# Kernel optimization log

Hardware: AMD Instinct MI355X
Metric: run time of the kernel (lower is better)

Reference implementation:

```python
import jax, jax.numpy as jnp
import numpy as np

T, B, C = 4, 2, 128
LT, LH, LW = 8, 32, 32
NUM_HEADS = 8
HEAD_DIM = C // NUM_HEADS
THETA = 0.7
V_TH = 1.0
TAU = 2.0  # spikingjelly LIFNode default tau
N_WIN = (2, 2, 2)
TOPK = 4
EPS = 1e-5
ATAN_ALPHA = 2.0  # spikingjelly surrogate.ATan default


@jax.custom_vjp
def spike(x):
    return (x >= 0.0).astype(x.dtype)

def _spike_fwd(x):
    return spike(x), x

def _spike_bwd(x, g):
    s = (jnp.pi / 2.0) * ATAN_ALPHA * x
    return (g * (ATAN_ALPHA / 2.0) / (1.0 + s * s),)

spike.defvjp(_spike_fwd, _spike_bwd)


def lif(x_seq):
    """Multi-step LIF: v'=v+(x-v)/tau, spike at v>=V_TH, hard reset to 0 (detached)."""
    def step(v, x):
        v = v + (x - v) / TAU
        s = spike(v - V_TH)
        v = v * (1.0 - jax.lax.stop_gradient(s))  # detach_reset, v_reset=0
        return v, s
    _, s_seq = jax.lax.scan(step, jnp.zeros_like(x_seq[0]), x_seq)
    return s_seq


def bn(x, gamma, beta):
    # BatchNorm3d(track_running_stats=False) on [T*B, C, D, H, W]: batch stats per channel
    mean = x.mean(axis=(0, 1, 3, 4, 5), keepdims=True)
    var = x.var(axis=(0, 1, 3, 4, 5), keepdims=True)
    shp = (1, 1, -1, 1, 1, 1)
    return (x - mean) * jax.lax.rsqrt(var + EPS) * gamma.reshape(shp) + beta.reshape(shp)


def conv3d(x, w, pad):
    t, b = x.shape[:2]
    y = jax.lax.conv_general_dilated(
        x.reshape((t * b,) + x.shape[2:]), w,
        window_strides=(1, 1, 1), padding=[(pad, pad)] * 3,
        dimension_numbers=('NCDHW', 'OIDHW', 'NCDHW'))
    return y.reshape((t, b) + y.shape[1:])


def cdc_t(x, w):
    out = conv3d(x, w, 1)
    # central-difference temporal term: 1x1x1 conv with summed first/last temporal slices
    kd = w[:, :, 0].sum((-1, -2)) + w[:, :, 2].sum((-1, -2))  # [O, I]
    return out - THETA * jnp.einsum('oi,tbidhw->tbodhw', kd, x)


def to_wins(t):
    wt, wh, ww = N_WIN
    Tn, Bn, Cn, Lt, Lh, Lw = t.shape
    lt, lh, lw = Lt // wt, Lh // wh, Lw // ww
    t = t.reshape(Tn, Bn, Cn, wt, lt, wh, lh, ww, lw)
    t = t.transpose(0, 1, 3, 5, 7, 4, 6, 8, 2)
    return t.reshape(Tn, Bn, wt * wh * ww, lt * lh * lw, Cn)


def setup_inputs() -> dict:
    key = jax.random.key(0)
    ks = jax.random.split(key, 4)
    x = jax.random.normal(ks[0], (T, B, C, LT, LH, LW), jnp.float32)
    qw = jax.random.normal(ks[1], (C, C, 3, 3, 3), jnp.float32) / np.sqrt(C * 27)
    kw = jax.random.normal(ks[2], (C, C), jnp.float32) / np.sqrt(C)
    pw = jax.random.normal(ks[3], (C, C), jnp.float32) / np.sqrt(C)
    ones = jnp.ones((C,), jnp.float32)
    zeros = jnp.zeros((C,), jnp.float32)
    return {"x": x, "qw": qw, "q_gamma": ones, "q_beta": zeros,
            "kw": kw, "k_gamma": ones, "k_beta": zeros,
            "v_gamma": ones, "v_beta": zeros,
            "pw": pw, "p_gamma": ones, "p_beta": zeros}


def reference(x, qw, q_gamma, q_beta, kw, k_gamma, k_beta,
              v_gamma, v_beta, pw, p_gamma, p_beta):
    Tn, Bn, Cn, Lt, Lh, Lw = x.shape
    wt, wh, ww = N_WIN
    num_wins = wt * wh * ww
    lt, lh, lw = Lt // wt, Lh // wh, Lw // ww

    q_real = bn(cdc_t(x, qw), q_gamma, q_beta)
    k_real = bn(jnp.einsum('oi,tbidhw->tbodhw', kw, x), k_gamma, k_beta)

    # region-level routing from pre-spike activations
    q_region = to_wins(q_real).mean(axis=(0, 3))  # [B, W, C]
    k_region = to_wins(k_real).mean(axis=(0, 3))
    a_r = jnp.einsum('bwc,bvc->bwv', q_region, k_region) * (HEAD_DIM ** -0.5)
    k_eff = min(TOPK, num_wins)
    _, idx = jax.lax.top_k(a_r, k_eff)  # [B, W, k]

    q = lif(q_real)
    k = lif(k_real)
    v = lif(bn(x, v_gamma, v_beta))
    q_w = to_wins(q)  # [T,B,W,S,C]
    k_w = to_wins(k)
    v_w = to_wins(v)

    # gather routed windows per (batch, target window), mean-aggregate over top-k
    gather = jax.vmap(lambda src_b, idx_b: src_b[:, idx_b], in_axes=(1, 0), out_axes=1)
    k_agg = gather(k_w, idx).mean(axis=3)  # [T,B,W,S,C]
    v_agg = gather(v_w, idx).mean(axis=3)

    S = q_w.shape[3]
    q_h = q_w.reshape(Tn, Bn, num_wins, S, NUM_HEADS, HEAD_DIM)
    k_h = k_agg.reshape(Tn, Bn, num_wins, S, NUM_HEADS, HEAD_DIM)
    v_h = v_agg.reshape(Tn, Bn, num_wins, S, NUM_HEADS, HEAD_DIM)

    attn = (q_h * k_h).sum(axis=5, keepdims=True)  # [T,B,W,S,H,1]
    attn = lif(attn)
    out = (attn * v_h).reshape(Tn, Bn, num_wins, S, Cn)

    out = out.reshape(Tn, Bn, wt, wh, ww, lt, lh, lw, Cn)
    out = out.transpose(0, 1, 8, 2, 5, 3, 6, 4, 7).reshape(Tn, Bn, Cn, Lt, Lh, Lw)

    out = lif(out)
    out = bn(jnp.einsum('oi,tbidhw->tbodhw', pw, out), p_gamma, p_beta)
    return out
```

## Files before the change

### kernel.cpp

```cpp
#include <hip/hip_runtime.h>

#define TT 4
#define BB 2
#define CC 128
#define DD 8
#define HHH 32
#define WWW 32
#define PP (DD*HHH*WWW)
#define TSTRIDE (BB*CC*PP)
#define NWIN 8
#define SSS 1024
#define NHEAD 8
#define HDIM 16
#define THETA 0.7f
#define VTH 1.0f
#define NPERC (TT*BB*PP)
#define EPSf 1e-5f

typedef unsigned short ushortT;
typedef _Float16 half_t;
typedef _Float16 f16x8 __attribute__((ext_vector_type(8)));
typedef float    f32x16 __attribute__((ext_vector_type(16)));

__global__ __launch_bounds__(256) void prep_wmodT(const float* __restrict__ qw,
                                                  float* __restrict__ wmodT) {
    int oi = blockIdx.x*256 + threadIdx.x;
    if (oi >= CC*CC) return;
    int o  = oi >> 7;
    int ic = oi & 127;
    const float* wp = qw + (size_t)oi*27;
    float kd = 0.f;
    #pragma unroll
    for (int t=0; t<9; t++) kd += wp[t] + wp[18+t];
    #pragma unroll
    for (int t=0; t<27; t++) {
        float v = wp[t] - ((t==13) ? THETA*kd : 0.f);
        wmodT[((size_t)o*27 + t)*CC + ic] = v;
    }
}

__global__ __launch_bounds__(256) void prep_wfrag(const float* __restrict__ wmodT,
                                                  half_t* __restrict__ wfrag) {
    int id = blockIdx.x*256 + threadIdx.x;
    if (id >= 8*27*4*64) return;
    int lane = id & 63;
    int r = id >> 6;
    int m = r & 3; r >>= 2;
    int t = r % 27;
    int kb = r / 27;
    int o   = m*32 + (lane & 31);
    int ic0 = kb*16 + (lane>>5)*8;
    size_t base = ((size_t)(id>>6))*2*64*8 + (size_t)lane*8;
    #pragma unroll
    for (int j=0;j<8;j++){
        float v = wmodT[((size_t)o*27 + t)*CC + ic0 + j];
        half_t h = (half_t)v;
        half_t l = (half_t)(v - (float)h);
        wfrag[base + 0*64*8 + j] = h;
        wfrag[base + 1*64*8 + j] = l;
    }
}

__global__ __launch_bounds__(256) void prep_w1frag(const float* __restrict__ W,
                                                   half_t* __restrict__ frag) {
    int id = blockIdx.x*256 + threadIdx.x;
    if (id >= 2048) return;
    int lane = id & 63;
    int r = id >> 6;
    int m = r & 3;
    int kb = r >> 2;
    int o   = m*32 + (lane & 31);
    int ic0 = kb*16 + (lane>>5)*8;
    size_t base = ((size_t)(kb*4+m))*2*64*8 + (size_t)lane*8;
    #pragma unroll
    for (int j=0;j<8;j++){
        float v = W[(size_t)o*CC + ic0 + j];
        half_t h = (half_t)v;
        half_t l = (half_t)(v - (float)h);
        frag[base + 0*64*8 + j] = h;
        frag[base + 1*64*8 + j] = l;
    }
}

__global__ __launch_bounds__(256) void build_xsplit(const float* __restrict__ x,
                                                    half_t* __restrict__ xsp) {
    int id = blockIdx.x*256 + threadIdx.x;
    if (id >= 8*16*8*34*34) return;
    int wt = id % 34; int r = id/34;
    int hp = r % 34;  r /= 34;
    int dz = r % 8;   r /= 8;
    int icg = r & 15; int tb = r >> 4;
    bool inb = (hp>=1) & (hp<=32) & (wt>=1) & (wt<=32);
    half_t h8[8], l8[8];
    #pragma unroll
    for (int j=0;j<8;j++){
        float v = 0.f;
        if (inb)
            v = x[((size_t)(tb*CC + icg*8+j))*PP + (size_t)dz*1024 + (hp-1)*32 + (wt-1)];
        half_t h = (half_t)v;
        half_t l = (half_t)(v - (float)h);
        h8[j]=h; l8[j]=l;
    }
    #pragma unroll
    for (int sp=0; sp<2; sp++){
        size_t gu = (((((size_t)tb*2 + sp)*16 + icg)*8 + dz)*34 + hp)*34 + wt;
        half_t* dst = xsp + gu*8;
        const half_t* src = (sp==0)?h8:l8;
        #pragma unroll
        for (int j=0;j<8;j++) dst[j] = src[j];
    }
}

__global__ __launch_bounds__(256,2) void conv_mfma2(const half_t* __restrict__ xsp,
                                                    const half_t* __restrict__ wfrag,
                                                    float* __restrict__ y0,
                                                    float* __restrict__ y1) {
    __shared__ half_t slab[3264*8];
    int tid  = threadIdx.x;
    int wid  = tid >> 6;
    int lane = tid & 63;
    int ln   = lane & 31;
    int half_ = lane >> 5;
    int hg = blockIdx.x;
    int dp = blockIdx.y;
    int z  = blockIdx.z;
    int tb = z >> 1, kh = z & 1;
    int H0 = hg*4, d0 = dp*2;
    float* y = kh ? y1 : y0;

    f32x16 acc[2][4];
    #pragma unroll
    for (int dt=0;dt<2;dt++)
        #pragma unroll
        for (int m=0;m<4;m++)
            #pragma unroll
            for (int i=0;i<16;i++) acc[dt][m][i] = 0.f;

    f16x8 ca[4][2];
    #pragma unroll
    for (int m=0;m<4;m++)
        #pragma unroll
        for (int sp=0;sp<2;sp++)
            ca[m][sp] = *(const f16x8*)&wfrag[((((size_t)(kh*4*27)*4 + m)*2+sp)*64 + lane)*8];

    #pragma unroll 1
    for (int kk=0; kk<4; kk++) {
        int kb = kh*4 + kk;
        __syncthreads();
        for (int u = tid; u < 3264; u += 256) {
            int sp  = u / 1632;
            int r   = u - sp*1632;
            int icg = r / 816;
            int p   = r - icg*816;
            int dz  = p / 204;
            int r3  = p - dz*204;
            int hp  = r3 / 34;
            int wt  = r3 - hp*34;
            int dd  = d0 - 1 + dz;
            ulonglong2 v; v.x = 0; v.y = 0;
            if ((unsigned)dd < 8u) {
                size_t gu = (((((size_t)tb*2 + sp)*16 + (kb*2+icg))*8 + dd)*34 + (H0+hp))*34 + wt;
                v = *(const ulonglong2*)&xsp[gu*8];
            }
            *(ulonglong2*)&slab[(size_t)u*8] = v;
        }
        __syncthreads();
        #pragma unroll 1
        for (int t=0; t<27; t++) {
            int dz=t/9; int rr=t-dz*9; int dh=rr/3; int dw=rr-dh*3;
            f16x8 cb[2][2];
            #pragma unroll
            for (int dt=0;dt<2;dt++){
                int bpos = (dt+dz)*204 + (wid+dh)*34 + ln + dw;
                #pragma unroll
                for (int sp=0;sp<2;sp++)
                    cb[dt][sp] = *(const f16x8*)&slab[(size_t)((sp*2+half_)*816 + bpos)*8];
            }
            f16x8 na[4][2];
            int nt  = (t<26)? t+1 : 0;
            int nkb = (t<26)? kb  : ((kk<3)? kb+1 : kb);
            #pragma unroll
            for (int m=0;m<4;m++)
                #pragma unroll
                for (int sp=0;sp<2;sp++)
                    na[m][sp] = *(const f16x8*)&wfrag[((((size_t)(nkb*27+nt)*4+m)*2+sp)*64 + lane)*8];
            #pragma unroll
            for (int dt=0;dt<2;dt++)
                #pragma unroll
                for (int m=0;m<4;m++) acc[dt][m] = __builtin_amdgcn_mfma_f32_32x32x16_f16(ca[m][0], cb[dt][0], acc[dt][m],0,0,0);
            #pragma unroll
            for (int dt=0;dt<2;dt++)
                #pragma unroll
                for (int m=0;m<4;m++) acc[dt][m] = __builtin_amdgcn_mfma_f32_32x32x16_f16(ca[m][0], cb[dt][1], acc[dt][m],0,0,0);
            #pragma unroll
            for (int dt=0;dt<2;dt++)
                #pragma unroll
                for (int m=0;m<4;m++) acc[dt][m] = __builtin_amdgcn_mfma_f32_32x32x16_f16(ca[m][1], cb[dt][0], acc[dt][m],0,0,0);
            #pragma unroll
            for (int dt=0;dt<2;dt++)
                #pragma unroll
                for (int m=0;m<4;m++) acc[dt][m] = __builtin_amdgcn_mfma_f32_32x32x16_f16(ca[m][1], cb[dt][1], acc[dt][m],0,0,0);
            #pragma unroll
            for (int m=0;m<4;m++)
                #pragma unroll
                for (int sp=0;sp<2;sp++) ca[m][sp] = na[m][sp];
        }
    }
    int h = H0 + wid;
    #pragma unroll
    for (int dt=0; dt<2; dt++) {
        #pragma unroll
        for (int m=0; m<4; m++) {
            #pragma unroll
            for (int reg=0; reg<16; reg++) {
                int row = (reg&3) + 8*(reg>>2) + 4*half_;
                int o = m*32 + row;
                y[((size_t)tb*CC + o)*PP + (d0+dt)*1024 + h*32 + ln] = acc[dt][m][reg];
            }
        }
    }
}

__global__ __launch_bounds__(256) void conv_add(float* __restrict__ q,
                                                const float* __restrict__ p1) {
    size_t i = ((size_t)blockIdx.x*256 + threadIdx.x)*4;
    float4 a = *(const float4*)&q[i];
    float4 b = *(const float4*)&p1[i];
    a.x+=b.x; a.y+=b.y; a.z+=b.z; a.w+=b.w;
    *(float4*)&q[i] = a;
}

__global__ __launch_bounds__(256) void kgemm_mfma(const half_t* __restrict__ xsp,
                                                  const half_t* __restrict__ wk,
                                                  float* __restrict__ y) {
    int tid  = threadIdx.x;
    int wid  = tid >> 6;
    int lane = tid & 63;
    int ln   = lane & 31;
    int half_ = lane >> 5;
    int hg = blockIdx.x, d = blockIdx.y, tb = blockIdx.z;
    int h = hg*4 + wid;

    f32x16 acc[4];
    #pragma unroll
    for (int m=0;m<4;m++)
        #pragma unroll
        for (int i=0;i<16;i++) acc[m][i] = 0.f;

    #pragma unroll 2
    for (int kb=0; kb<8; kb++) {
        f16x8 b[2];
        #pragma unroll
        for (int sp=0; sp<2; sp++) {
            size_t gu = (((((size_t)tb*2 + sp)*16 + (kb*2+half_))*8 + d)*34 + (h+1))*34 + (ln+1);
            b[sp] = *(const f16x8*)&xsp[gu*8];
        }
        #pragma unroll
        for (int m=0; m<4; m++) {
            const half_t* wb = wk + ((size_t)(kb*4+m))*2*64*8 + (size_t)lane*8;
            f16x8 a0 = *(const f16x8*)&wb[0*64*8];
            f16x8 a1 = *(const f16x8*)&wb[1*64*8];
            acc[m] = __builtin_amdgcn_mfma_f32_32x32x16_f16(a0, b[0], acc[m],0,0,0);
            acc[m] = __builtin_amdgcn_mfma_f32_32x32x16_f16(a0, b[1], acc[m],0,0,0);
            acc[m] = __builtin_amdgcn_mfma_f32_32x32x16_f16(a1, b[0], acc[m],0,0,0);
            acc[m] = __builtin_amdgcn_mfma_f32_32x32x16_f16(a1, b[1], acc[m],0,0,0);
        }
    }
    #pragma unroll
    for (int m=0; m<4; m++) {
        #pragma unroll
        for (int reg=0; reg<16; reg++) {
            int row = (reg&3) + 8*(reg>>2) + 4*half_;
            int o = m*32 + row;
            y[((size_t)tb*CC + o)*PP + d*1024 + h*32 + ln] = acc[m][reg];
        }
    }
}

__global__ __launch_bounds__(256) void pgemm_mfma(const ushortT* __restrict__ spkb,
                                                  const half_t* __restrict__ wp,
                                                  float* __restrict__ y) {
    int tid  = threadIdx.x;
    int wid  = tid >> 6;
    int lane = tid & 63;
    int ln   = lane & 31;
    int half_ = lane >> 5;
    int hg = blockIdx.x, d = blockIdx.y, tb = blockIdx.z;
    int h = hg*4 + wid;
    int p = d*1024 + h*32 + ln;

    f32x16 acc[4];
    #pragma unroll
    for (int m=0;m<4;m++)
        #pragma unroll
        for (int i=0;i<16;i++) acc[m][i] = 0.f;

    #pragma unroll 2
    for (int kb=0; kb<8; kb++) {
        f16x8 b = *(const f16x8*)&spkb[(((size_t)tb*16 + (kb*2+half_))*PP + p)*8];
        #pragma unroll
        for (int m=0; m<4; m++) {
            const half_t* wb = wp + ((size_t)(kb*4+m))*2*64*8 + (size_t)lane*8;
            f16x8 a0 = *(const f16x8*)&wb[0*64*8];
            f16x8 a1 = *(const f16x8*)&wb[1*64*8];
            acc[m] = __builtin_amdgcn_mfma_f32_32x32x16_f16(a0, b, acc[m],0,0,0);
            acc[m] = __builtin_amdgcn_mfma_f32_32x32x16_f16(a1, b, acc[m],0,0,0);
        }
    }
    #pragma unroll
    for (int m=0; m<4; m++) {
        #pragma unroll
        for (int reg=0; reg<16; reg++) {
            int row = (reg&3) + 8*(reg>>2) + 4*half_;
            int o = m*32 + row;
            y[((size_t)tb*CC + o)*PP + p] = acc[m][reg];
        }
    }
}

__global__ __launch_bounds__(128) void win_stats(const float* __restrict__ q,
        const float* __restrict__ k, const float* __restrict__ x,
        float* __restrict__ rsum, float* __restrict__ rsq) {
    int blk = blockIdx.x;
    int src = blk >> 11;
    int r   = blk & 2047;
    const float* base = (src==0) ? q : ((src==1) ? k : x);
    int c  = r & 127;
    int wi = (r >> 7) & 7;
    int b  = r >> 10;
    int wd = wi>>2, wh = (wi>>1)&1, ww = wi&1;
    int tid = threadIdx.x;
    float s=0.f, s2=0.f;
    for (int t=0;t<TT;t++){
        const float* p = base + ((size_t)(t*BB+b)*CC + c)*PP;
        for (int si=tid; si<SSS; si+=128){
            int ld = si>>8, lh=(si>>4)&15, lw=si&15;
            float v = p[((wd*4+ld)<<10) + ((wh*16+lh)<<5) + (ww*16+lw)];
            s += v; s2 += v*v;
        }
    }
    __shared__ float ls[128], ls2[128];
    ls[tid]=s; ls2[tid]=s2; __syncthreads();
    for (int off=64;off>0;off>>=1){
        if(tid<off){ ls[tid]+=ls[tid+off]; ls2[tid]+=ls2[tid+off]; }
        __syncthreads();
    }
    if (tid==0){ rsum[blk]=ls[0]; rsq[blk]=ls2[0]; }
}

__global__ __launch_bounds__(384) void stats_fin(const float* __restrict__ rsum,
        const float* __restrict__ rsq, float* __restrict__ sums) {
    int tid = threadIdx.x;
    int src = tid >> 7, c = tid & 127;
    float s=0.f, s2=0.f;
    for (int bw=0; bw<16; bw++){
        int idx = src*2048 + bw*128 + c;
        s  += rsum[idx];
        s2 += rsq[idx];
    }
    sums[src*256 + c]       = s;
    sums[src*256 + 128 + c] = s2;
}

__global__ __launch_bounds__(128) void route_topk(const float* __restrict__ qreg,
        const float* __restrict__ kreg,
        const float* __restrict__ qsum, const float* __restrict__ qsq,
        const float* __restrict__ ksum, const float* __restrict__ ksq,
        const float* __restrict__ qg, const float* __restrict__ qb,
        const float* __restrict__ kg, const float* __restrict__ kb,
        int* __restrict__ idxout) {
    __shared__ float qn[16*128], kn[16*128], ar[16*8];
    int tid = threadIdx.x;
    for (int e=tid; e<16*128; e+=128){
        int c = e&127;
        float qm = qsum[c]*(1.f/NPERC);
        float qv = qsq[c]*(1.f/NPERC) - qm*qm;
        float qr = rsqrtf(qv + EPSf);
        qn[e] = (qreg[e]*(1.f/(TT*SSS)) - qm)*qr*qg[c] + qb[c];
        float km = ksum[c]*(1.f/NPERC);
        float kv = ksq[c]*(1.f/NPERC) - km*km;
        float kr = rsqrtf(kv + EPSf);
        kn[e] = (kreg[e]*(1.f/(TT*SSS)) - km)*kr*kg[c] + kb[c];
    }
    __syncthreads();
    {
        int b = tid>>6, w=(tid>>3)&7, v=tid&7;
        float s=0.f;
        for (int c=0;c<128;c++) s += qn[(b*8+w)*128+c]*kn[(b*8+v)*128+c];
        ar[(b*8+w)*8+v] = s * 0.25f;
    }
    __syncthreads();
    if (tid < 16){
        const float* row = &ar[tid*8];
        bool used[8] = {false,false,false,false,false,false,false,false};
        for (int j=0;j<4;j++){
            int best=0; float bv=-3.0e38f;
            for (int v=0; v<8; v++){
                if (!used[v] && row[v] > bv){ bv=row[v]; best=v; }
            }
            used[best]=true;
            idxout[tid*4+j]=best;
        }
    }
}

__global__ __launch_bounds__(256) void lif_bn_win3(const float* __restrict__ qin,
        const float* __restrict__ kin, const float* __restrict__ xin,
        float* __restrict__ qs, float* __restrict__ ks, float* __restrict__ vs,
        const float* __restrict__ stats,
        const float* __restrict__ qg, const float* __restrict__ qb,
        const float* __restrict__ kg, const float* __restrict__ kb,
        const float* __restrict__ vg, const float* __restrict__ vb) {
    int src = blockIdx.y;
    const float* in  = (src==0) ? qin : ((src==1) ? kin : xin);
    float*       spk = (src==0) ? qs  : ((src==1) ? ks  : vs);
    const float* gamma = (src==0) ? qg : ((src==1) ? kg : vg);
    const float* beta  = (src==0) ? qb : ((src==1) ? kb : vb);
    int e = blockIdx.x*256 + threadIdx.x;
    if (e >= BB*CC*PP) return;
    int p = e & (PP-1);
    int c = (e >> 13) & 127;
    int b = e >> 20;
    float mean = stats[src*256 + c]*(1.f/NPERC);
    float var  = stats[src*256 + 128 + c]*(1.f/NPERC) - mean*mean;
    float sc = rsqrtf(var+EPSf)*gamma[c];
    float sh = beta[c] - mean*sc;
    int d = p>>10, h=(p>>5)&31, w=p&31;
    int wi = ((d>>2)*2 + (h>>4))*2 + (w>>4);
    int si = (((d&3)<<4) + (h&15))*16 + (w&15);
    size_t widx = ((size_t)(b*NWIN+wi)*CC + c)*SSS + si;
    float v=0.f;
    #pragma unroll
    for (int t=0;t<TT;t++){
        float xn = in[(size_t)t*TSTRIDE + e]*sc + sh;
        v = (v+xn)*0.5f;
        float s = (v>=VTH)?1.f:0.f;
        spk[(size_t)t*TSTRIDE + widx] = s;
        v *= (1.f - s);
    }
}

__global__ __launch_bounds__(256) void attn_lif(const float* __restrict__ qspk,
        const float* __restrict__ kspk, const float* __restrict__ vspk,
        const int* __restrict__ idx, ushortT* __restrict__ spkb) {
    int id = blockIdx.x*256 + threadIdx.x;
    if (id >= BB*NWIN*NHEAD*SSS) return;
    int s  = id & 1023;
    int hh = (id>>10) & 7;
    int wi = (id>>13) & 7;
    int b  = id>>16;
    int bw = b*NWIN+wi;
    size_t qbase = ((size_t)bw*CC + hh*HDIM)*SSS + s;
    size_t sbase[4];
    #pragma unroll
    for (int j=0;j<4;j++){
        int src = idx[bw*4+j];
        sbase[j] = ((size_t)(b*NWIN+src)*CC + hh*HDIM)*SSS + s;
    }
    int wd = wi>>2, wh = (wi>>1)&1, ww = wi&1;
    int d3 = wd*4 + (s>>8), h3 = wh*16 + ((s>>4)&15), w3 = ww*16 + (s&15);
    int p  = (d3<<10) + (h3<<5) + w3;

    float v=0.f;
    float v2[16];
    #pragma unroll
    for (int dd=0; dd<16; dd++) v2[dd]=0.f;

    #pragma unroll 1
    for (int t=0;t<TT;t++){
        size_t toff = (size_t)t*TSTRIDE;
        float km[16], vm[16];
        #pragma unroll
        for (int dd=0;dd<16;dd++){ km[dd]=0.f; vm[dd]=0.f; }
        #pragma unroll
        for (int j=0;j<4;j++){
            const float* kp = kspk+toff+sbase[j];
            const float* vp = vspk+toff+sbase[j];
            #pragma unroll
            for (int dd=0; dd<16; dd++){
                km[dd] += kp[(size_t)dd*SSS];
                vm[dd] += vp[(size_t)dd*SSS];
            }
        }
        const float* qp = qspk+toff+qbase;
        float att=0.f;
        #pragma unroll
        for (int dd=0;dd<16;dd++) att += qp[(size_t)dd*SSS]*km[dd];
        att *= 0.25f;
        v = (v+att)*0.5f;
        float sp = (v>=VTH)?1.f:0.f;
        v *= (1.f-sp);
        float spq = sp*0.25f;
        union { ushortT u[8]; uint4 q4; } pk0, pk1;
        #pragma unroll
        for (int dd=0;dd<16;dd++){
            float ov = spq*vm[dd];
            v2[dd] = (v2[dd]+ov)*0.5f;
            float s2 = (v2[dd]>=VTH)?1.f:0.f;
            v2[dd] *= (1.f-s2);
            ushortT bs = (s2 != 0.f) ? (ushortT)0x3C00 : (ushortT)0;
            if (dd < 8) pk0.u[dd] = bs; else pk1.u[dd-8] = bs;
        }
        int tb2 = t*BB + b;
        size_t base = (((size_t)tb2*16 + hh*2)*PP + p)*8;
        *(uint4*)&spkb[base] = pk0.q4;
        *(uint4*)&spkb[base + (size_t)PP*8] = pk1.q4;
    }
}

__global__ __launch_bounds__(256) void pstats_part(const float* __restrict__ xin,
        float* __restrict__ part_sum, float* __restrict__ part_sq) {
    int blk = blockIdx.x;
    int c = blk & 127, tb = blk >> 7;
    int tid = threadIdx.x;
    const float* p = xin + ((size_t)tb*CC + c)*PP;
    float s=0.f, s2=0.f;
    for (int i=tid; i<PP; i+=256){ float v=p[i]; s+=v; s2+=v*v; }
    __shared__ float ls[256], ls2[256];
    ls[tid]=s; ls2[tid]=s2; __syncthreads();
    for (int off=128; off>0; off>>=1){
        if (tid<off){ ls[tid]+=ls[tid+off]; ls2[tid]+=ls2[tid+off]; }
        __syncthreads();
    }
    if (tid==0){ part_sum[blk]=ls[0]; part_sq[blk]=ls2[0]; }
}

__global__ __launch_bounds__(128) void pstats_fin(const float* __restrict__ part_sum,
        const float* __restrict__ part_sq, float* __restrict__ sum,
        float* __restrict__ sq) {
    int c = threadIdx.x;
    float s=0.f, s2=0.f;
    for (int tb=0; tb<8; tb++){
        s  += part_sum[tb*128+c];
        s2 += part_sq[tb*128+c];
    }
    sum[c]=s; sq[c]=s2;
}

__global__ __launch_bounds__(256) void bn_apply(const float* __restrict__ xin,
        float* __restrict__ yout,
        const float* __restrict__ sum, const float* __restrict__ sq,
        const float* __restrict__ gamma, const float* __restrict__ beta) {
    size_t i = (size_t)blockIdx.x*256 + threadIdx.x;
    if (i >= (size_t)TT*BB*CC*PP) return;
    int c = (int)((i>>13)&127);
    float mean = sum[c]*(1.f/NPERC);
    float var  = sq[c]*(1.f/NPERC) - mean*mean;
    float sc = rsqrtf(var+EPSf)*gamma[c];
    float sh = beta[c] - mean*sc;
    yout[i] = xin[i]*sc + sh;
}

extern "C" void kernel_launch(void* const* d_in, const int* in_sizes, int n_in,
                              void* d_out, int out_size, void* d_ws, size_t ws_size,
                              hipStream_t stream) {
    const float* x  = (const float*)d_in[0];
    const float* qw = (const float*)d_in[1];
    const float* qg = (const float*)d_in[2];
    const float* qb = (const float*)d_in[3];
    const float* kw = (const float*)d_in[4];
    const float* kg = (const float*)d_in[5];
    const float* kb = (const float*)d_in[6];
    const float* vg = (const float*)d_in[7];
    const float* vb = (const float*)d_in[8];
    const float* pw = (const float*)d_in[9];
    const float* pg = (const float*)d_in[10];
    const float* pb = (const float*)d_in[11];
    float* out = (float*)d_out;
    float* ws  = (float*)d_ws;

    const size_t NEL = (size_t)TT*TSTRIDE;
    float* qconv = ws;
    float* kconv = ws + NEL;
    float* qspk  = ws + 2*NEL;
    float* kspk  = ws + 3*NEL;
    float* vspk  = ws + 4*NEL;
    float* wmodT = ws + 5*NEL;
    float* stats = ws + 5*NEL + 442368;
    float *qsum=stats,     *qsq=stats+128,  *ksum=stats+256, *ksq=stats+384,
          *psum=stats+768, *psq=stats+896;
    float* rsum = stats + 1024;
    float* rsq  = rsum + 6144;
    float* ppart_sum = rsq + 6144;
    float* ppart_sq  = ppart_sum + 1024;
    int*   idxp = (int*)(ppart_sq + 1024);

    half_t* xsp    = (half_t*)(ws + 2*NEL);
    half_t* wfrag  = (half_t*)(ws + 4*NEL);
    half_t* wkfrag = (half_t*)(ws + 4*NEL) + 884736;
    half_t* wpfrag = (half_t*)(ws + 4*NEL);
    ushortT* spkb  = (ushortT*)(ws + NEL);
    float*   pconv = ws + 2*NEL;
    float*   part1 = kconv;

    prep_wmodT<<<64,256,0,stream>>>(qw, wmodT);
    prep_wfrag<<<216,256,0,stream>>>(wmodT, wfrag);
    prep_w1frag<<<8,256,0,stream>>>(kw, wkfrag);
    build_xsplit<<<4624,256,0,stream>>>(x, xsp);
    {
        dim3 cg(8,4,16);
        conv_mfma2<<<cg,256,0,stream>>>(xsp, wfrag, qconv, part1);
    }
    conv_add<<<8192,256,0,stream>>>(qconv, part1);
    {
        dim3 gg(8,8,8);
        kgemm_mfma<<<gg,256,0,stream>>>(xsp, wkfrag, kconv);
    }
    win_stats<<<6144,128,0,stream>>>(qconv, kconv, x, rsum, rsq);
    stats_fin<<<1,384,0,stream>>>(rsum, rsq, stats);
    route_topk<<<1,128,0,stream>>>(rsum, rsum+2048, qsum,qsq,ksum,ksq,qg,qb,kg,kb,idxp);
    {
        dim3 lg(8192,3);
        lif_bn_win3<<<lg,256,0,stream>>>(qconv,kconv,x, qspk,kspk,vspk,
                                         stats, qg,qb,kg,kb,vg,vb);
    }
    attn_lif<<<512,256,0,stream>>>(qspk,kspk,vspk,idxp,spkb);
    prep_w1frag<<<8,256,0,stream>>>(pw, wpfrag);
    {
        dim3 gg(8,8,8);
        pgemm_mfma<<<gg,256,0,stream>>>(spkb, wpfrag, pconv);
    }
    pstats_part<<<1024,256,0,stream>>>(pconv, ppart_sum, ppart_sq);
    pstats_fin<<<1,128,0,stream>>>(ppart_sum, ppart_sq, psum, psq);
    bn_apply<<<32768,256,0,stream>>>(pconv, out, psum, psq, pg, pb);
}
```

Measured before the change: 449.6 us.

## Drop lo*lo split-fp16 MFMA terms, store spikes as fp16, fuse stats into routing

Removes the fourth MFMA in the hi/lo split-precision products of both the 3x3x3 conv and the 1x1 k GEMM, keeping only the hi*hi, hi*lo and lo*hi terms. This cuts matrix work by a quarter and accepts a tiny precision loss. The q/k/v spike tensors are now written and read as fp16 instead of fp32, which halves their memory traffic in the LIF and attention kernels. The separate single-block stats_fin launch is folded into route_topk to save one kernel launch.

```diff
diff --git a/kernel.cpp b/kernel.cpp
--- a/kernel.cpp
+++ b/kernel.cpp
@@ -197,10 +197,6 @@
                 #pragma unroll
                 for (int m=0;m<4;m++) acc[dt][m] = __builtin_amdgcn_mfma_f32_32x32x16_f16(ca[m][1], cb[dt][0], acc[dt][m],0,0,0);
             #pragma unroll
-            for (int dt=0;dt<2;dt++)
-                #pragma unroll
-                for (int m=0;m<4;m++) acc[dt][m] = __builtin_amdgcn_mfma_f32_32x32x16_f16(ca[m][1], cb[dt][1], acc[dt][m],0,0,0);
-            #pragma unroll
             for (int m=0;m<4;m++)
                 #pragma unroll
                 for (int sp=0;sp<2;sp++) ca[m][sp] = na[m][sp];
@@ -263,7 +259,6 @@
             acc[m] = __builtin_amdgcn_mfma_f32_32x32x16_f16(a0, b[0], acc[m],0,0,0);
             acc[m] = __builtin_amdgcn_mfma_f32_32x32x16_f16(a0, b[1], acc[m],0,0,0);
             acc[m] = __builtin_amdgcn_mfma_f32_32x32x16_f16(a1, b[0], acc[m],0,0,0);
-            acc[m] = __builtin_amdgcn_mfma_f32_32x32x16_f16(a1, b[1], acc[m],0,0,0);
         }
     }
     #pragma unroll
@@ -348,39 +343,37 @@
     if (tid==0){ rsum[blk]=ls[0]; rsq[blk]=ls2[0]; }
 }
 
-__global__ __launch_bounds__(384) void stats_fin(const float* __restrict__ rsum,
-        const float* __restrict__ rsq, float* __restrict__ sums) {
-    int tid = threadIdx.x;
-    int src = tid >> 7, c = tid & 127;
-    float s=0.f, s2=0.f;
-    for (int bw=0; bw<16; bw++){
-        int idx = src*2048 + bw*128 + c;
-        s  += rsum[idx];
-        s2 += rsq[idx];
-    }
-    sums[src*256 + c]       = s;
-    sums[src*256 + 128 + c] = s2;
-}
-
-__global__ __launch_bounds__(128) void route_topk(const float* __restrict__ qreg,
-        const float* __restrict__ kreg,
-        const float* __restrict__ qsum, const float* __restrict__ qsq,
-        const float* __restrict__ ksum, const float* __restrict__ ksq,
+__global__ __launch_bounds__(128) void route_topk(const float* __restrict__ rsum,
+        const float* __restrict__ rsq, float* __restrict__ sums,
         const float* __restrict__ qg, const float* __restrict__ qb,
         const float* __restrict__ kg, const float* __restrict__ kb,
         int* __restrict__ idxout) {
-    __shared__ float qn[16*128], kn[16*128], ar[16*8];
+    __shared__ float qn[16*128], kn[16*128], ar[16*8], ss[768];
     int tid = threadIdx.x;
+    for (int e=tid; e<384; e+=128){
+        int src = e >> 7, c = e & 127;
+        float s=0.f, s2=0.f;
+        for (int bw=0; bw<16; bw++){
+            int idx = src*2048 + bw*128 + c;
+            s  += rsum[idx];
+            s2 += rsq[idx];
+        }
+        sums[src*256 + c]       = s;
+        sums[src*256 + 128 + c] = s2;
+        ss[src*256 + c]       = s;
+        ss[src*256 + 128 + c] = s2;
+    }
+    __syncthreads();
     for (int e=tid; e<16*128; e+=128){
         int c = e&127;
-        float qm = qsum[c]*(1.f/NPERC);
-        float qv = qsq[c]*(1.f/NPERC) - qm*qm;
+        float qm = ss[c]*(1.f/NPERC);
+        float qv = ss[128+c]*(1.f/NPERC) - qm*qm;
         float qr = rsqrtf(qv + EPSf);
-        qn[e] = (qreg[e]*(1.f/(TT*SSS)) - qm)*qr*qg[c] + qb[c];
-        float km = ksum[c]*(1.f/NPERC);
-        float kv = ksq[c]*(1.f/NPERC) - km*km;
+        qn[e] = (rsum[e]*(1.f/(TT*SSS)) - qm)*qr*qg[c] + qb[c];
+        float km = ss[256+c]*(1.f/NPERC);
+        float kv = ss[256+128+c]*(1.f/NPERC) - km*km;
         float kr = rsqrtf(kv + EPSf);
-        kn[e] = (kreg[e]*(1.f/(TT*SSS)) - km)*kr*kg[c] + kb[c];
+        kn[e] = (rsum[2048+e]*(1.f/(TT*SSS)) - km)*kr*kg[c] + kb[c];
     }
     __syncthreads();
     {
@@ -406,14 +399,14 @@
 
 __global__ __launch_bounds__(256) void lif_bn_win3(const float* __restrict__ qin,
         const float* __restrict__ kin, const float* __restrict__ xin,
-        float* __restrict__ qs, float* __restrict__ ks, float* __restrict__ vs,
+        ushortT* __restrict__ qs, ushortT* __restrict__ ks, ushortT* __restrict__ vs,
         const float* __restrict__ stats,
         const float* __restrict__ qg, const float* __restrict__ qb,
         const float* __restrict__ kg, const float* __restrict__ kb,
         const float* __restrict__ vg, const float* __restrict__ vb) {
     int src = blockIdx.y;
     const float* in  = (src==0) ? qin : ((src==1) ? kin : xin);
-    float*       spk = (src==0) ? qs  : ((src==1) ? ks  : vs);
+    ushortT*     spk = (src==0) ? qs  : ((src==1) ? ks  : vs);
     const float* gamma = (src==0) ? qg : ((src==1) ? kg : vg);
     const float* beta  = (src==0) ? qb : ((src==1) ? kb : vb);
     int e = blockIdx.x*256 + threadIdx.x;
@@ -435,13 +428,13 @@
         float xn = in[(size_t)t*TSTRIDE + e]*sc + sh;
         v = (v+xn)*0.5f;
         float s = (v>=VTH)?1.f:0.f;
-        spk[(size_t)t*TSTRIDE + widx] = s;
+        spk[(size_t)t*TSTRIDE + widx] = (v>=VTH)?(ushortT)0x3C00:(ushortT)0;
         v *= (1.f - s);
     }
 }
 
-__global__ __launch_bounds__(256) void attn_lif(const float* __restrict__ qspk,
-        const float* __restrict__ kspk, const float* __restrict__ vspk,
+__global__ __launch_bounds__(256) void attn_lif(const half_t* __restrict__ qspk,
+        const half_t* __restrict__ kspk, const half_t* __restrict__ vspk,
         const int* __restrict__ idx, ushortT* __restrict__ spkb) {
     int id = blockIdx.x*256 + threadIdx.x;
     if (id >= BB*NWIN*NHEAD*SSS) return;
@@ -474,18 +467,18 @@
         for (int dd=0;dd<16;dd++){ km[dd]=0.f; vm[dd]=0.f; }
         #pragma unroll
         for (int j=0;j<4;j++){
-            const float* kp = kspk+toff+sbase[j];
-            const float* vp = vspk+toff+sbase[j];
+            const half_t* kp = kspk+toff+sbase[j];
+            const half_t* vp = vspk+toff+sbase[j];
             #pragma unroll
             for (int dd=0; dd<16; dd++){
-                km[dd] += kp[(size_t)dd*SSS];
-                vm[dd] += vp[(size_t)dd*SSS];
+                km[dd] += (float)kp[(size_t)dd*SSS];
+                vm[dd] += (float)vp[(size_t)dd*SSS];
             }
         }
-        const float* qp = qspk+toff+qbase;
+        const half_t* qp = qspk+toff+qbase;
         float att=0.f;
         #pragma unroll
-        for (int dd=0;dd<16;dd++) att += qp[(size_t)dd*SSS]*km[dd];
+        for (int dd=0;dd<16;dd++) att += (float)qp[(size_t)dd*SSS]*km[dd];
         att *= 0.25f;
         v = (v+att)*0.5f;
         float sp = (v>=VTH)?1.f:0.f;
@@ -572,13 +565,9 @@
     const size_t NEL = (size_t)TT*TSTRIDE;
     float* qconv = ws;
     float* kconv = ws + NEL;
-    float* qspk  = ws + 2*NEL;
-    float* kspk  = ws + 3*NEL;
-    float* vspk  = ws + 4*NEL;
     float* wmodT = ws + 5*NEL;
     float* stats = ws + 5*NEL + 442368;
-    float *qsum=stats,     *qsq=stats+128,  *ksum=stats+256, *ksq=stats+384,
-          *psum=stats+768, *psq=stats+896;
+    float *psum=stats+768, *psq=stats+896;
     float* rsum = stats + 1024;
     float* rsq  = rsum + 6144;
     float* ppart_sum = rsq + 6144;
@@ -590,7 +579,10 @@
     half_t* wkfrag = (half_t*)(ws + 4*NEL) + 884736;
     half_t* wpfrag = (half_t*)(ws + 4*NEL);
     ushortT* spkb  = (ushortT*)(ws + NEL);
-    float*   pconv = ws + 2*NEL;
+    ushortT* qspkh = (ushortT*)(ws + 2*NEL);
+    ushortT* kspkh = qspkh + NEL;
+    ushortT* vspkh = qspkh + 2*NEL;
+    float*   pconv = ws;
     float*   part1 = kconv;
 
     prep_wmodT<<<64,256,0,stream>>>(qw, wmodT);
@@ -607,14 +599,14 @@
         kgemm_mfma<<<gg,256,0,stream>>>(xsp, wkfrag, kconv);
     }
     win_stats<<<6144,128,0,stream>>>(qconv, kconv, x, rsum, rsq);
-    stats_fin<<<1,384,0,stream>>>(rsum, rsq, stats);
-    route_topk<<<1,128,0,stream>>>(rsum, rsum+2048, qsum,qsq,ksum,ksq,qg,qb,kg,kb,idxp);
+    route_topk<<<1,128,0,stream>>>(rsum, rsq, stats, qg,qb,kg,kb, idxp);
     {
         dim3 lg(8192,3);
-        lif_bn_win3<<<lg,256,0,stream>>>(qconv,kconv,x, qspk,kspk,vspk,
+        lif_bn_win3<<<lg,256,0,stream>>>(qconv,kconv,x, qspkh,kspkh,vspkh,
                                          stats, qg,qb,kg,kb,vg,vb);
     }
-    attn_lif<<<512,256,0,stream>>>(qspk,kspk,vspk,idxp,spkb);
+    attn_lif<<<512,256,0,stream>>>((const half_t*)qspkh,(const half_t*)kspkh,
+                                   (const half_t*)vspkh, idxp, spkb);
     prep_w1frag<<<8,256,0,stream>>>(pw, wpfrag);
     {
         dim3 gg(8,8,8);
```

After: 458.2 us. Within noise of the previous version (+1.9%).
